# Optimization experiments

Hardware: AMD Instinct MI355X
Metric: run time of the kernel (lower is better)

## Reference

```python
import jax, jax.numpy as jnp
import numpy as np

B, N, D, H = 16, 4096, 768, 16
E = D // H  # head dim = 48
EPS = 1e-12  # F.normalize eps


def setup_inputs() -> dict:
    key = jax.random.key(0)
    ks = jax.random.split(key, 10)
    s = 0.02
    return {
        "x": jax.random.normal(ks[0], (B, N, D), dtype=jnp.float32),
        "wq": jax.random.normal(ks[1], (D, D), dtype=jnp.float32) * s,
        "bq": jnp.zeros((D,), dtype=jnp.float32),
        "wk": jax.random.normal(ks[2], (D, D), dtype=jnp.float32) * s,
        "bk": jnp.zeros((D,), dtype=jnp.float32),
        "wv": jax.random.normal(ks[3], (D, D), dtype=jnp.float32) * s,
        "bv": jnp.zeros((D,), dtype=jnp.float32),
        "wo": jax.random.normal(ks[4], (D, D), dtype=jnp.float32) * s,
        "bo": jnp.zeros((D,), dtype=jnp.float32),
        "tau": jnp.float32(H),  # scalar learnable temperature, init = num_heads
    }


def _l2norm_seq(t):
    # F.normalize(t, p=2, dim=1): normalize over sequence axis n of [b, n, h, e]
    nrm = jnp.sqrt(jnp.sum(t * t, axis=1, keepdims=True))
    return t / jnp.maximum(nrm, EPS)


def reference(x, wq, bq, wk, bk, wv, bv, wo, bo, tau):
    b, n, d = x.shape
    q = (x @ wq.T + bq).reshape(b, n, H, E)
    k = (x @ wk.T + bk).reshape(b, n, H, E)
    v = (x @ wv.T + bv).reshape(b, n, H, E)
    q = _l2norm_seq(q)
    k = _l2norm_seq(k)
    # cross-covariance attention over feature dim: [b, e, h, q]
    energy = jnp.einsum('bnhe,bnhq->behq', q, k)
    attn = jax.nn.softmax(energy, axis=-1)
    out = jnp.einsum('behq,bnhe->bnhq', attn / tau, v)  # [b, n, h, e]
    out = out.reshape(b, n, d)
    return out @ wo.T + bo
```

## Files before the change

kernel.cpp:

```cpp
#include <hip/hip_runtime.h>
#include <hip/hip_bf16.h>

typedef __attribute__((ext_vector_type(8))) short bf16x8_t;
typedef __attribute__((ext_vector_type(4))) float f32x4_t;
typedef __attribute__((ext_vector_type(4))) float fv4;
typedef __attribute__((ext_vector_type(4))) unsigned short us4_t;
typedef __attribute__((ext_vector_type(8))) unsigned short us8_t;

static constexpr int BB = 16, NN = 4096, DD = 768, HH = 16, EE = 48;

__device__ __forceinline__ unsigned short f2bf(float f) {
  unsigned int u = __float_as_uint(f);
  u += 0x7fffu + ((u >> 16) & 1u);
  return (unsigned short)(u >> 16);
}
__device__ __forceinline__ float bf2f(unsigned short s) {
  unsigned int u = ((unsigned int)s) << 16;
  return __uint_as_float(u);
}

__device__ __forceinline__ void load_lds16(const void* g, void* l) {
  __builtin_amdgcn_global_load_lds((const __attribute__((address_space(1))) void*)g,
                                   (__attribute__((address_space(3))) void*)l, 16, 0, 0);
}

template<int WRITE_THRU>
__device__ __forceinline__ void tcast64(const float* __restrict__ src, int sld,
                                        unsigned short* __restrict__ dst, int dld,
                                        unsigned short* __restrict__ thru, int tld, int t)
{
  __shared__ float L[64][65];
#pragma unroll
  for (int q = 0; q < 4; ++q) {
    const int fi = t + q * 256;
    const int r = fi >> 4, c4 = fi & 15;
    fv4 v = *(const fv4*)(src + (long)r * sld + c4 * 4);
    L[r][c4 * 4 + 0] = v.x; L[r][c4 * 4 + 1] = v.y;
    L[r][c4 * 4 + 2] = v.z; L[r][c4 * 4 + 3] = v.w;
    if (WRITE_THRU) {
      us4_t o; o.x = f2bf(v.x); o.y = f2bf(v.y); o.z = f2bf(v.z); o.w = f2bf(v.w);
      *(us4_t*)(thru + (long)r * tld + c4 * 4) = o;
    }
  }
  __syncthreads();
#pragma unroll
  for (int q = 0; q < 2; ++q) {
    const int wi = t + q * 256;
    const int rr = wi >> 3, ng = wi & 7;
    us8_t o;
#pragma unroll
    for (int j = 0; j < 8; ++j) o[j] = f2bf(L[ng * 8 + j][rr]);
    *(us8_t*)(dst + (long)rr * dld + ng * 8) = o;
  }
  __syncthreads();
}

__global__ __launch_bounds__(256) void transpose_cast_x(
    const float* __restrict__ x, unsigned short* __restrict__ xb,
    unsigned short* __restrict__ xbT)
{
  const int nx = blockIdx.x, dx = blockIdx.y, b = blockIdx.z;
  const int n0 = nx * 64, d0 = dx * 64;
  const float* src = x + ((long)b * NN + n0) * DD + d0;
  unsigned short* thru = xb + ((long)b * NN + n0) * DD + d0;
  unsigned short* dst = xbT + ((long)b * DD + d0) * NN + n0;
  tcast64<1>(src, DD, dst, NN, thru, DD, threadIdx.x);
}

__global__ __launch_bounds__(256) void small_cast(
    const float* __restrict__ wq, const float* __restrict__ wk, const float* __restrict__ wv,
    unsigned short* __restrict__ W2, unsigned short* __restrict__ wvT,
    float* __restrict__ zeros)
{
  const int blk = blockIdx.x, t = threadIdx.x;
  if (blk < 576) {
#pragma unroll
    for (int q = 0; q < 2; ++q) {
      long g = (long)blk * 512 + t * 2 + q;
      long e0 = g * 4;
      int row = (int)(e0 / DD), col = (int)(e0 % DD);
      const float* src = (row < DD) ? (wq + (long)row * DD + col)
                                    : (wk + (long)(row - DD) * DD + col);
      fv4 v = *(const fv4*)src;
      us4_t o; o.x = f2bf(v.x); o.y = f2bf(v.y); o.z = f2bf(v.z); o.w = f2bf(v.w);
      *(us4_t*)(W2 + e0) = o;
    }
  } else if (blk < 720) {
    const int tile = blk - 576;
    const int ti = tile / 12, tj = tile % 12;
    const int k0 = ti * 64, i0 = tj * 64;
    tcast64<0>(wv + (long)i0 * DD + k0, DD, wvT + (long)k0 * DD + i0, DD, nullptr, 0, t);
  } else {
#pragma unroll
    for (int q = 0; q < 4; ++q) zeros[t * 4 + q] = 0.f;
  }
}

__global__ __launch_bounds__(256) void colsum(
    const unsigned short* __restrict__ xbT, float* __restrict__ xsum)
{
  const int bx = blockIdx.x, b = blockIdx.y;
  const int wave = threadIdx.x >> 6, lane = threadIdx.x & 63;
  const int d = bx * 4 + wave;
  const unsigned short* row = xbT + ((long)b * DD + d) * NN;
  float s = 0.f;
#pragma unroll
  for (int it = 0; it < 8; ++it) {
    us8_t v = *(const us8_t*)(row + (it * 64 + lane) * 8);
#pragma unroll
    for (int j = 0; j < 8; ++j) s += bf2f(v[j]);
  }
#pragma unroll
  for (int off = 32; off > 0; off >>= 1) s += __shfl_down(s, off);
  if (lane == 0) xsum[(long)b * DD + d] = s;
}

template<int OUT_BF16, int SYM>
__global__ __launch_bounds__(256) void gemm_bt(
    const unsigned short* __restrict__ A, int lda, long aStride,
    const unsigned short* __restrict__ Bt, int ldb, long bStride,
    void* __restrict__ Cv, int ldc, long cStride,
    const float* __restrict__ bias, long biasStride, int K,
    int perB, int nt)
{
  __shared__ unsigned short As[128 * 64];
  __shared__ unsigned short Bs[128 * 64];
  const int nwg = gridDim.x;
  const int bid = blockIdx.x;
  const int wid = (bid & 7) * (nwg >> 3) + (bid >> 3);
  const int zb = wid / perB;
  const int t0 = wid % perB;
  int i0, j0;
  if (SYM) {
    int tt = t0; i0 = 0;
    while (tt >= nt - i0) { tt -= nt - i0; ++i0; }
    j0 = i0 + tt;
  } else {
    i0 = t0 / nt; j0 = t0 % nt;
  }
  const unsigned short* Ab = A + (long)zb * aStride;
  const unsigned short* Bb = Bt + (long)zb * bStride;
  const float* bz = bias + (long)zb * biasStride;
  const long m0 = (long)i0 * 128;
  const int n0 = j0 * 128;
  const int t = threadIdx.x;
  const int wave = t >> 6, lane = t & 63;
  const int wr = wave >> 1, wc = wave & 1;

  f32x4_t acc[4][4] = {};

  const int srow = t >> 3;
  const long scol = (long)(((t & 7) ^ (srow & 7)) << 3);
  unsigned short* ldsA = As + wave * 512;
  unsigned short* ldsB = Bs + wave * 512;

  for (int kt = 0; kt < K; kt += 64) {
#pragma unroll
    for (int p = 0; p < 4; ++p) {
      load_lds16(Ab + (m0 + p * 32 + srow) * (long)lda + kt + scol, ldsA + p * 2048);
      load_lds16(Bb + (long)(n0 + p * 32 + srow) * ldb + kt + scol, ldsB + p * 2048);
    }
    __syncthreads();
#pragma unroll
    for (int kk = 0; kk < 2; ++kk) {
      const int cswz = (((kk << 2) + (lane >> 4)) ^ (lane & 7)) << 4;
      bf16x8_t af[4], bfr[4];
#pragma unroll
      for (int f = 0; f < 4; ++f) {
        af[f]  = *(const bf16x8_t*)((const char*)As + (wr * 64 + f * 16 + (lane & 15)) * 128 + cswz);
        bfr[f] = *(const bf16x8_t*)((const char*)Bs + (wc * 64 + f * 16 + (lane & 15)) * 128 + cswz);
      }
#pragma unroll
      for (int i = 0; i < 4; ++i)
#pragma unroll
        for (int j = 0; j < 4; ++j)
          acc[i][j] = __builtin_amdgcn_mfma_f32_16x16x32_bf16(af[i], bfr[j], acc[i][j], 0, 0, 0);
    }
    __syncthreads();
  }

  const int col_l = lane & 15;
  const int rbase = (lane >> 4) << 2;
#pragma unroll
  for (int i = 0; i < 4; ++i) {
    const long growb = m0 + wr * 64 + i * 16 + rbase;
#pragma unroll
    for (int j = 0; j < 4; ++j) {
      const int col = n0 + wc * 64 + j * 16 + col_l;
      if (OUT_BF16) {
        const float bcol = bz[col];
        us4_t o;
#pragma unroll
        for (int r = 0; r < 4; ++r) o[r] = f2bf(acc[i][j][r] + bcol);
        unsigned short* cb = (unsigned short*)Cv + (long)zb * cStride;
#pragma unroll
        for (int r = 0; r < 4; ++r) cb[(growb + r) * ldc + col] = o[r];
        if (SYM && i0 != j0)
          *(us4_t*)(cb + (long)col * ldc + growb) = o;
      } else {
#pragma unroll
        for (int r = 0; r < 4; ++r) {
          float* crow = (float*)Cv + (long)zb * cStride + (growb + r) * ldc;
          crow[col] = acc[i][j][r] + bz[col];
        }
      }
    }
  }
}

#define GP_STRIDE 2464

__global__ __launch_bounds__(256) void energy_partial2(
    const unsigned short* __restrict__ T, const unsigned short* __restrict__ W2,
    float* __restrict__ Gp)
{
  __shared__ unsigned short Ts[2][48 * 128];
  __shared__ unsigned short Ws[2][48 * 128];
  __shared__ float G_sh[2448];

  const int kc = blockIdx.x, h = blockIdx.y, b = blockIdx.z;
  const int t = threadIdx.x;
  const int wave = t >> 6, lane = t & 63;

  for (int i = t; i < 2448; i += 256) G_sh[i] = 0.f;

  f32x4_t accG[3][3] = {};
  f32x4_t accQ[3] = {};
  f32x4_t accK[3] = {};

  long qoff[3];
#pragma unroll
  for (int p = 0; p < 3; ++p) {
    const int L = p * 4096 + wave * 1024 + lane * 16;
    const int e = L >> 8;
    const int blk = (L >> 4) & 15;
    const int sblk = blk ^ (e & 7);
    qoff[p] = (long)e * DD + sblk * 8;
  }
  const unsigned short* Tq = T + ((long)b * 1536 + h * 48) * DD;
  const unsigned short* Tk = Tq + (long)DD * DD;
  const unsigned short* Wq = W2 + (long)h * 48 * DD;
  const unsigned short* Wk = Wq + (long)DD * DD;

  int foff[3];
#pragma unroll
  for (int f = 0; f < 3; ++f) {
    const int e = f * 16 + (lane & 15);
    foff[f] = e * 256 + (((wave * 4 + (lane >> 4)) ^ (e & 7)) << 4);
  }
  __syncthreads();

  for (int ci = 0; ci < 3; ++ci) {
    const int col0 = kc * 384 + ci * 128;
#pragma unroll
    for (int p = 0; p < 3; ++p) {
      load_lds16(Tq + qoff[p] + col0, &Ts[0][p * 2048] + wave * 512);
      load_lds16(Tk + qoff[p] + col0, &Ts[1][p * 2048] + wave * 512);
      load_lds16(Wq + qoff[p] + col0, &Ws[0][p * 2048] + wave * 512);
      load_lds16(Wk + qoff[p] + col0, &Ws[1][p * 2048] + wave * 512);
    }
    __syncthreads();
    bf16x8_t tq[3], tk[3], wqf[3], wkf[3];
#pragma unroll
    for (int f = 0; f < 3; ++f) {
      tq[f]  = *(const bf16x8_t*)((const char*)&Ts[0][0] + foff[f]);
      tk[f]  = *(const bf16x8_t*)((const char*)&Ts[1][0] + foff[f]);
      wqf[f] = *(const bf16x8_t*)((const char*)&Ws[0][0] + foff[f]);
      wkf[f] = *(const bf16x8_t*)((const char*)&Ws[1][0] + foff[f]);
    }
#pragma unroll
    for (int i = 0; i < 3; ++i) {
      accQ[i] = __builtin_amdgcn_mfma_f32_16x16x32_bf16(tq[i], wqf[i], accQ[i], 0, 0, 0);
      accK[i] = __builtin_amdgcn_mfma_f32_16x16x32_bf16(tk[i], wkf[i], accK[i], 0, 0, 0);
#pragma unroll
      for (int j = 0; j < 3; ++j)
        accG[i][j] = __builtin_amdgcn_mfma_f32_16x16x32_bf16(tq[i], wkf[j], accG[i][j], 0, 0, 0);
    }
    __syncthreads();
  }

#pragma unroll
  for (int i = 0; i < 3; ++i)
#pragma unroll
    for (int j = 0; j < 3; ++j) {
      int e = i * 16 + ((lane >> 4) << 2);
      int qi = j * 16 + (lane & 15);
#pragma unroll
      for (int r = 0; r < 4; ++r) atomicAdd(&G_sh[(e + r) * 49 + qi], accG[i][j][r]);
    }
  if ((lane >> 4) == ((lane & 15) >> 2)) {
    int r = (lane & 15) & 3;
#pragma unroll
    for (int f = 0; f < 3; ++f) {
      atomicAdd(&G_sh[2352 + f * 16 + (lane & 15)], accQ[f][r]);
      atomicAdd(&G_sh[2400 + f * 16 + (lane & 15)], accK[f][r]);
    }
  }
  __syncthreads();

  float* out = Gp + (long)(((b * HH + h) << 1) + kc) * GP_STRIDE;
  for (int i = t; i < 2448; i += 256) out[i] = G_sh[i];
}

__global__ __launch_bounds__(256) void energy_finish2(
    const float* __restrict__ Gp, const float* __restrict__ xsum,
    const float* __restrict__ wq, const float* __restrict__ wk,
    const float* __restrict__ bq, const float* __restrict__ bk,
    const float* __restrict__ tau_p, unsigned short* __restrict__ A_out)
{
  __shared__ float G_sh[2448];
  __shared__ float vq[48], vk[48], bqs[48], bks[48];
  __shared__ int has_bias;
  const int h = blockIdx.x, b = blockIdx.y;
  const int t = threadIdx.x;

  const float* base = Gp + (long)((b * HH + h) << 1) * GP_STRIDE;
  for (int i = t; i < 2448; i += 256)
    G_sh[i] = base[i] + base[GP_STRIDE + i];
  if (t < 48) { bqs[t] = bq[h * 48 + t]; bks[t] = bk[h * 48 + t]; }
  __syncthreads();
  if (t == 0) {
    float s = 0.f;
    for (int i = 0; i < 48; ++i) s += fabsf(bqs[i]) + fabsf(bks[i]);
    has_bias = (s != 0.f);
  }
  __syncthreads();
  if (has_bias) {
    if (t < 96) {
      const int e = t < 48 ? t : t - 48;
      const float* wrow = (t < 48 ? wq : wk) + (long)(h * 48 + e) * DD;
      const float* xs = xsum + (long)b * DD;
      float s = 0.f;
      for (int g = 0; g < DD / 4; ++g) {
        fv4 a = *(const fv4*)(wrow + g * 4);
        fv4 c = *(const fv4*)(xs + g * 4);
        s += a.x * c.x + a.y * c.y + a.z * c.z + a.w * c.w;
      }
      if (t < 48) vq[e] = s; else vk[e] = s;
    }
  } else if (t < 48) { vq[t] = 0.f; vk[t] = 0.f; }
  __syncthreads();

  if (t < 48) {
    const float tau = *tau_p;
    const float nq2c = G_sh[2352 + t] + 2.f * bqs[t] * vq[t] + (float)NN * bqs[t] * bqs[t];
    const float nq = fmaxf(sqrtf(nq2c), 1e-12f);
    float row[48];
    float mx = -1e30f;
#pragma unroll 1
    for (int qi = 0; qi < 48; ++qi) {
      float nk2c = G_sh[2400 + qi] + 2.f * bks[qi] * vk[qi] + (float)NN * bks[qi] * bks[qi];
      float nk = fmaxf(sqrtf(nk2c), 1e-12f);
      float e = G_sh[t * 49 + qi] + vq[t] * bks[qi] + bqs[t] * vk[qi]
              + (float)NN * bqs[t] * bks[qi];
      float g = e / (nq * nk);
      row[qi] = g; mx = fmaxf(mx, g);
    }
    float s = 0.f;
#pragma unroll 1
    for (int qi = 0; qi < 48; ++qi) { row[qi] = __expf(row[qi] - mx); s += row[qi]; }
    const float inv = 1.f / (s * tau);
    unsigned short* dst = A_out + (((long)b * HH + h) * 48) * 64 + (long)t * 64;
#pragma unroll 1
    for (int qi = 0; qi < 48; ++qi) dst[qi] = f2bf(row[qi] * inv);
#pragma unroll 1
    for (int qi = 48; qi < 64; ++qi) dst[qi] = 0;
  }
}

__global__ __launch_bounds__(256) void build_btf(
    const unsigned short* __restrict__ A_ws, const float* __restrict__ wo,
    unsigned short* __restrict__ btf)
{
  __shared__ unsigned short Wsh[128 * 72];
  __shared__ unsigned short Ash[48 * 72];
  const int nchunk = blockIdx.x, h = blockIdx.y, b = blockIdx.z;
  const int t = threadIdx.x;
  const int wave = t >> 6, lane = t & 63;
  const int no0 = nchunk * 128;

  for (int i = t; i < 128 * 64; i += 256) {
    int r = i >> 6, c = i & 63;
    Wsh[r * 72 + c] = (c < 48) ? f2bf(wo[(long)(no0 + r) * DD + h * 48 + c]) : (unsigned short)0;
  }
  const unsigned short* Asrc = A_ws + ((long)b * HH + h) * 48 * 64;
  for (int i = t; i < 48 * 64; i += 256) {
    int r = i >> 6, c = i & 63;
    Ash[r * 72 + c] = Asrc[r * 64 + c];
  }
  __syncthreads();

  f32x4_t acc[2][3] = {};
#pragma unroll
  for (int ks = 0; ks < 2; ++ks) {
    const int k0 = ks * 32 + ((lane >> 4) << 3);
    bf16x8_t af[2], bfr[3];
#pragma unroll
    for (int mi = 0; mi < 2; ++mi)
      af[mi] = *(const bf16x8_t*)&Wsh[(wave * 32 + mi * 16 + (lane & 15)) * 72 + k0];
#pragma unroll
    for (int nj = 0; nj < 3; ++nj)
      bfr[nj] = *(const bf16x8_t*)&Ash[(nj * 16 + (lane & 15)) * 72 + k0];
#pragma unroll
    for (int mi = 0; mi < 2; ++mi)
#pragma unroll
      for (int nj = 0; nj < 3; ++nj)
        acc[mi][nj] = __builtin_amdgcn_mfma_f32_16x16x32_bf16(af[mi], bfr[nj], acc[mi][nj], 0, 0, 0);
  }

  const int col_l = lane & 15;
  const int rbase = (lane >> 4) << 2;
#pragma unroll
  for (int mi = 0; mi < 2; ++mi)
#pragma unroll
    for (int r = 0; r < 4; ++r) {
      int no = no0 + wave * 32 + mi * 16 + rbase + r;
      unsigned short* dst = btf + ((long)b * DD + no) * DD + h * 48;
#pragma unroll
      for (int nj = 0; nj < 3; ++nj)
        dst[nj * 16 + col_l] = f2bf(acc[mi][nj][r]);
    }
}

__global__ __launch_bounds__(256) void build_bias2(
    const unsigned short* __restrict__ btf, const float* __restrict__ bv,
    const float* __restrict__ bo, float* __restrict__ bias2)
{
  const int bx = blockIdx.x, b = blockIdx.y;
  const int wave = threadIdx.x >> 6, lane = threadIdx.x & 63;
  const int j = bx * 4 + wave;
  const unsigned short* row = btf + ((long)b * DD + j) * DD;
  float s = 0.f;
#pragma unroll
  for (int ii = 0; ii < 12; ++ii) {
    int i = ii * 64 + lane;
    s += bf2f(row[i]) * bv[i];
  }
#pragma unroll
  for (int off = 32; off > 0; off >>= 1) s += __shfl_down(s, off);
  if (lane == 0) bias2[(long)b * DD + j] = bo[j] + s;
}

extern "C" void kernel_launch(void* const* d_in, const int* in_sizes, int n_in,
                              void* d_out, int out_size, void* d_ws, size_t ws_size,
                              hipStream_t stream)
{
  (void)in_sizes; (void)n_in; (void)out_size;
  const float* x   = (const float*)d_in[0];
  const float* wq  = (const float*)d_in[1];
  const float* bq  = (const float*)d_in[2];
  const float* wk  = (const float*)d_in[3];
  const float* bk  = (const float*)d_in[4];
  const float* wv  = (const float*)d_in[5];
  const float* bv  = (const float*)d_in[6];
  const float* wo  = (const float*)d_in[7];
  const float* bo  = (const float*)d_in[8];
  const float* tau = (const float*)d_in[9];

  char* ws = (char*)d_ws;
  unsigned short* xb    = (unsigned short*)(ws + 0L);
  unsigned short* xbT   = (unsigned short*)(ws + 100663296L);
  unsigned short* S     = (unsigned short*)(ws + 201326592L);
  unsigned short* T     = (unsigned short*)(ws + 220200960L);
  unsigned short* W2    = (unsigned short*)(ws + 257949696L);
  unsigned short* wvT   = (unsigned short*)(ws + 260308992L);
  float*          zeros = (float*)         (ws + 261488640L);
  float*          xsum  = (float*)         (ws + 261492736L);
  float*          Gp    = (float*)         (ws + 261541888L);
  unsigned short* A_ws  = (unsigned short*)(ws + 266588160L);
  unsigned short* btf   = (unsigned short*)(ws + 268161024L);
  unsigned short* Ctf   = (unsigned short*)(ws + 287035392L);
  float*          bias2 = (float*)         (ws + 305909760L);
  if (ws_size < 305958912ULL) return;

  transpose_cast_x<<<dim3(64, 12, BB), 256, 0, stream>>>(x, xb, xbT);
  small_cast<<<721, 256, 0, stream>>>(wq, wk, wv, W2, wvT, zeros);
  colsum<<<dim3(192, BB), 256, 0, stream>>>(xbT, xsum);

  gemm_bt<1, 1><<<16 * 21, 256, 0, stream>>>(
      xbT, NN, (long)DD * NN, xbT, NN, (long)DD * NN,
      S, DD, (long)DD * DD, zeros, 0L, NN, 21, 6);

  gemm_bt<1, 0><<<16 * 72, 256, 0, stream>>>(
      W2, DD, 0L, S, DD, (long)DD * DD,
      T, DD, (long)1536 * DD, zeros, 0L, DD, 72, 6);

  energy_partial2<<<dim3(2, HH, BB), 256, 0, stream>>>(T, W2, Gp);
  energy_finish2<<<dim3(HH, BB), 256, 0, stream>>>(Gp, xsum, wq, wk, bq, bk, tau, A_ws);

  build_btf<<<dim3(6, HH, BB), 256, 0, stream>>>(A_ws, wo, btf);
  build_bias2<<<dim3(192, BB), 256, 0, stream>>>(btf, bv, bo, bias2);

  gemm_bt<1, 0><<<16 * 36, 256, 0, stream>>>(
      btf, DD, (long)DD * DD, wvT, DD, 0L,
      Ctf, DD, (long)DD * DD, zeros, 0L, DD, 36, 6);

  gemm_bt<0, 0><<<16 * 192, 256, 0, stream>>>(
      xb, DD, (long)NN * DD, Ctf, DD, (long)DD * DD,
      d_out, DD, (long)NN * DD, bias2, (long)DD, DD, 192, 6);
}
```

Baseline: 484.2 us.

## Split-K the Gram GEMM and fuse column sums into the x transpose

The symmetric X^T X Gram GEMM (K=4096, only 336 tiles) is split into two K halves, doubling the workgroup count. Each half writes fp32 partials, and a new reduce_s kernel adds them, casts to bf16 and mirrors each tile into the symmetric half of S. Separately, the standalone colsum kernel is removed: column sums of x are now built in transpose_cast_x through shared-memory and global atomics, with small_cast zeroing xsum first. This trades extra fp32 partial traffic, one extra launch and atomics for better GPU occupancy on the Gram GEMM and one fewer pass over xbT.

```diff
diff --git a/kernel.cpp b/kernel.cpp
--- a/kernel.cpp
+++ b/kernel.cpp
@@ -24,10 +24,8 @@
                                    (__attribute__((address_space(3))) void*)l, 16, 0, 0);
 }
 
-template<int WRITE_THRU>
 __device__ __forceinline__ void tcast64(const float* __restrict__ src, int sld,
-                                        unsigned short* __restrict__ dst, int dld,
-                                        unsigned short* __restrict__ thru, int tld, int t)
+                                        unsigned short* __restrict__ dst, int dld, int t)
 {
   __shared__ float L[64][65];
 #pragma unroll
@@ -37,10 +35,6 @@
     fv4 v = *(const fv4*)(src + (long)r * sld + c4 * 4);
     L[r][c4 * 4 + 0] = v.x; L[r][c4 * 4 + 1] = v.y;
     L[r][c4 * 4 + 2] = v.z; L[r][c4 * 4 + 3] = v.w;
-    if (WRITE_THRU) {
-      us4_t o; o.x = f2bf(v.x); o.y = f2bf(v.y); o.z = f2bf(v.z); o.w = f2bf(v.w);
-      *(us4_t*)(thru + (long)r * tld + c4 * 4) = o;
-    }
   }
   __syncthreads();
 #pragma unroll
@@ -57,20 +51,46 @@
 
 __global__ __launch_bounds__(256) void transpose_cast_x(
     const float* __restrict__ x, unsigned short* __restrict__ xb,
-    unsigned short* __restrict__ xbT)
-{
+    unsigned short* __restrict__ xbT, float* __restrict__ xsum)
+{
+  __shared__ float L[64][65];
+  __shared__ float csum[64];
   const int nx = blockIdx.x, dx = blockIdx.y, b = blockIdx.z;
   const int n0 = nx * 64, d0 = dx * 64;
+  const int t = threadIdx.x;
+  if (t < 64) csum[t] = 0.f;
   const float* src = x + ((long)b * NN + n0) * DD + d0;
   unsigned short* thru = xb + ((long)b * NN + n0) * DD + d0;
   unsigned short* dst = xbT + ((long)b * DD + d0) * NN + n0;
-  tcast64<1>(src, DD, dst, NN, thru, DD, threadIdx.x);
+#pragma unroll
+  for (int q = 0; q < 4; ++q) {
+    const int fi = t + q * 256;
+    const int r = fi >> 4, c4 = fi & 15;
+    fv4 v = *(const fv4*)(src + (long)r * DD + c4 * 4);
+    L[r][c4 * 4 + 0] = v.x; L[r][c4 * 4 + 1] = v.y;
+    L[r][c4 * 4 + 2] = v.z; L[r][c4 * 4 + 3] = v.w;
+    us4_t o; o.x = f2bf(v.x); o.y = f2bf(v.y); o.z = f2bf(v.z); o.w = f2bf(v.w);
+    *(us4_t*)(thru + (long)r * DD + c4 * 4) = o;
+  }
+  __syncthreads();
+#pragma unroll
+  for (int q = 0; q < 2; ++q) {
+    const int wi = t + q * 256;
+    const int rr = wi >> 3, ng = wi & 7;
+    us8_t o; float s8 = 0.f;
+#pragma unroll
+    for (int j = 0; j < 8; ++j) { float v = L[ng * 8 + j][rr]; o[j] = f2bf(v); s8 += v; }
+    *(us8_t*)(dst + (long)rr * NN + ng * 8) = o;
+    atomicAdd(&csum[rr], s8);
+  }
+  __syncthreads();
+  if (t < 64) atomicAdd(&xsum[(long)b * DD + d0 + t], csum[t]);
 }
 
 __global__ __launch_bounds__(256) void small_cast(
     const float* __restrict__ wq, const float* __restrict__ wk, const float* __restrict__ wv,
     unsigned short* __restrict__ W2, unsigned short* __restrict__ wvT,
-    float* __restrict__ zeros)
+    float* __restrict__ zeros, float* __restrict__ xsum)
 {
   const int blk = blockIdx.x, t = threadIdx.x;
   if (blk < 576) {
@@ -89,38 +109,22 @@
     const int tile = blk - 576;
     const int ti = tile / 12, tj = tile % 12;
     const int k0 = ti * 64, i0 = tj * 64;
-    tcast64<0>(wv + (long)i0 * DD + k0, DD, wvT + (long)k0 * DD + i0, DD, nullptr, 0, t);
+    tcast64(wv + (long)i0 * DD + k0, DD, wvT + (long)k0 * DD + i0, DD, t);
+  } else if (blk == 720) {
+#pragma unroll
+    for (int q = 0; q < 4; ++q) zeros[t * 4 + q] = 0.f;
   } else {
 #pragma unroll
-    for (int q = 0; q < 4; ++q) zeros[t * 4 + q] = 0.f;
-  }
-}
-
-__global__ __launch_bounds__(256) void colsum(
-    const unsigned short* __restrict__ xbT, float* __restrict__ xsum)
-{
-  const int bx = blockIdx.x, b = blockIdx.y;
-  const int wave = threadIdx.x >> 6, lane = threadIdx.x & 63;
-  const int d = bx * 4 + wave;
-  const unsigned short* row = xbT + ((long)b * DD + d) * NN;
-  float s = 0.f;
-#pragma unroll
-  for (int it = 0; it < 8; ++it) {
-    us8_t v = *(const us8_t*)(row + (it * 64 + lane) * 8);
-#pragma unroll
-    for (int j = 0; j < 8; ++j) s += bf2f(v[j]);
-  }
-#pragma unroll
-  for (int off = 32; off > 0; off >>= 1) s += __shfl_down(s, off);
-  if (lane == 0) xsum[(long)b * DD + d] = s;
+    for (int q = 0; q < 4; ++q) xsum[(long)(blk - 721) * 1024 + t * 4 + q] = 0.f;
+  }
 }
 
 template<int OUT_BF16, int SYM>
 __global__ __launch_bounds__(256) void gemm_bt(
     const unsigned short* __restrict__ A, int lda, long aStride,
     const unsigned short* __restrict__ Bt, int ldb, long bStride,
-    void* __restrict__ Cv, int ldc, long cStride,
-    const float* __restrict__ bias, long biasStride, int K,
+    void* __restrict__ Cv, int ldc, long cStride, long cHalfStride,
+    const float* __restrict__ bias, long biasStride, int K, int kSplit,
     int perB, int nt)
 {
   __shared__ unsigned short As[128 * 64];
@@ -128,8 +132,11 @@
   const int nwg = gridDim.x;
   const int bid = blockIdx.x;
   const int wid = (bid & 7) * (nwg >> 3) + (bid >> 3);
-  const int zb = wid / perB;
+  const int zb2 = wid / perB;
   const int t0 = wid % perB;
+  const int zb = zb2 / kSplit;
+  const int half = zb2 - zb * kSplit;
+  const int kOff = half * K;
   int i0, j0;
   if (SYM) {
     int tt = t0; i0 = 0;
@@ -154,7 +161,7 @@
   unsigned short* ldsA = As + wave * 512;
   unsigned short* ldsB = Bs + wave * 512;
 
-  for (int kt = 0; kt < K; kt += 64) {
+  for (int kt = kOff; kt < kOff + K; kt += 64) {
 #pragma unroll
     for (int p = 0; p < 4; ++p) {
       load_lds16(Ab + (m0 + p * 32 + srow) * (long)lda + kt + scol, ldsA + p * 2048);
@@ -198,13 +205,55 @@
         if (SYM && i0 != j0)
           *(us4_t*)(cb + (long)col * ldc + growb) = o;
       } else {
-#pragma unroll
-        for (int r = 0; r < 4; ++r) {
-          float* crow = (float*)Cv + (long)zb * cStride + (growb + r) * ldc;
-          crow[col] = acc[i][j][r] + bz[col];
-        }
+        float* cbase = (float*)Cv + (long)half * cHalfStride + (long)zb * cStride;
+#pragma unroll
+        for (int r = 0; r < 4; ++r)
+          cbase[(growb + r) * ldc + col] = acc[i][j][r] + bz[col];
       }
     }
+  }
+}
+
+__global__ __launch_bounds__(256) void reduce_s(
+    const float* __restrict__ P, unsigned short* __restrict__ S)
+{
+  __shared__ float L[64][65];
+  const int t0 = blockIdx.x, b = blockIdx.y;
+  int tt = t0, i0 = 0;
+  while (tt >= 6 - i0) { tt -= 6 - i0; ++i0; }
+  const int j0 = i0 + tt;
+  const int t = threadIdx.x;
+  const float* P0 = P + (long)b * 589824;
+  const float* P1 = P0 + 9437184L;
+  unsigned short* Sb = S + (long)b * 589824;
+#pragma unroll
+  for (int st = 0; st < 4; ++st) {
+    const int m0 = i0 * 128 + (st >> 1) * 64;
+    const int n0 = j0 * 128 + (st & 1) * 64;
+#pragma unroll
+    for (int q = 0; q < 4; ++q) {
+      const int fi = t + q * 256;
+      const int r = fi >> 4, c4 = fi & 15;
+      const long off = (long)(m0 + r) * DD + n0 + c4 * 4;
+      fv4 a = *(const fv4*)(P0 + off);
+      fv4 c = *(const fv4*)(P1 + off);
+      fv4 s; s.x = a.x + c.x; s.y = a.y + c.y; s.z = a.z + c.z; s.w = a.w + c.w;
+      L[r][c4 * 4 + 0] = s.x; L[r][c4 * 4 + 1] = s.y;
+      L[r][c4 * 4 + 2] = s.z; L[r][c4 * 4 + 3] = s.w;
+      us4_t o; o.x = f2bf(s.x); o.y = f2bf(s.y); o.z = f2bf(s.z); o.w = f2bf(s.w);
+      *(us4_t*)(Sb + off) = o;
+    }
+    __syncthreads();
+#pragma unroll
+    for (int q = 0; q < 2; ++q) {
+      const int wi = t + q * 256;
+      const int rr = wi >> 3, ng = wi & 7;
+      us8_t o;
+#pragma unroll
+      for (int j = 0; j < 8; ++j) o[j] = f2bf(L[ng * 8 + j][rr]);
+      *(us8_t*)(Sb + (long)(n0 + rr) * DD + m0 + ng * 8) = o;
+    }
+    __syncthreads();
   }
 }
 
@@ -471,19 +520,20 @@
   unsigned short* btf   = (unsigned short*)(ws + 268161024L);
   unsigned short* Ctf   = (unsigned short*)(ws + 287035392L);
   float*          bias2 = (float*)         (ws + 305909760L);
-  if (ws_size < 305958912ULL) return;
-
-  transpose_cast_x<<<dim3(64, 12, BB), 256, 0, stream>>>(x, xb, xbT);
-  small_cast<<<721, 256, 0, stream>>>(wq, wk, wv, W2, wvT, zeros);
-  colsum<<<dim3(192, BB), 256, 0, stream>>>(xbT, xsum);
-
-  gemm_bt<1, 1><<<16 * 21, 256, 0, stream>>>(
+  float*          Pbuf  = (float*)         (ws + 305958912L);
+  if (ws_size < 381456384ULL) return;
+
+  small_cast<<<733, 256, 0, stream>>>(wq, wk, wv, W2, wvT, zeros, xsum);
+  transpose_cast_x<<<dim3(64, 12, BB), 256, 0, stream>>>(x, xb, xbT, xsum);
+
+  gemm_bt<0, 1><<<16 * 2 * 21, 256, 0, stream>>>(
       xbT, NN, (long)DD * NN, xbT, NN, (long)DD * NN,
-      S, DD, (long)DD * DD, zeros, 0L, NN, 21, 6);
+      Pbuf, DD, 589824L, 9437184L, zeros, 0L, 2048, 2, 21, 6);
+  reduce_s<<<dim3(21, BB), 256, 0, stream>>>(Pbuf, S);
 
   gemm_bt<1, 0><<<16 * 72, 256, 0, stream>>>(
       W2, DD, 0L, S, DD, (long)DD * DD,
-      T, DD, (long)1536 * DD, zeros, 0L, DD, 72, 6);
+      T, DD, (long)1536 * DD, 0L, zeros, 0L, DD, 1, 72, 6);
 
   energy_partial2<<<dim3(2, HH, BB), 256, 0, stream>>>(T, W2, Gp);
   energy_finish2<<<dim3(HH, BB), 256, 0, stream>>>(Gp, xsum, wq, wk, bq, bk, tau, A_ws);
@@ -493,9 +543,9 @@
 
   gemm_bt<1, 0><<<16 * 36, 256, 0, stream>>>(
       btf, DD, (long)DD * DD, wvT, DD, 0L,
-      Ctf, DD, (long)DD * DD, zeros, 0L, DD, 36, 6);
+      Ctf, DD, (long)DD * DD, 0L, zeros, 0L, DD, 1, 36, 6);
 
   gemm_bt<0, 0><<<16 * 192, 256, 0, stream>>>(
       xb, DD, (long)NN * DD, Ctf, DD, (long)DD * DD,
-      d_out, DD, (long)NN * DD, bias2, (long)DD, DD, 192, 6);
-}
+      d_out, DD, (long)NN * DD, 0L, bias2, (long)DD, DD, 1, 192, 6);
+}
```

Measured after the change: 493.2 us. Within noise of the previous version (+1.9%).
